# Optimization experiments

Measured on AMD Instinct MI355X. Metric: run time of the kernel, lower is better.

The kernel has to match this reference:

```python
import jax, jax.numpy as jnp
import numpy as np

NEG = -1000.0  # matches the -1000 masking used in the original module


def setup_inputs() -> dict:
    key = jax.random.key(0)
    k0, k1, k2 = jax.random.split(key, 3)
    B, L, T = 512, 512, 32
    S = T + 2  # states: 0 = START, 1..T = tags, T+1 = STOP
    word_tag_value = jax.random.normal(k0, (B, L, T), dtype=jnp.float32)
    # xavier_uniform-style init for the transition matrix, then mask per the original
    a = float(np.sqrt(6.0 / (S + S)))
    translation = jax.random.uniform(k1, (S, S), dtype=jnp.float32, minval=-a, maxval=a)
    translation = translation.at[:, 0].set(NEG)       # nothing transitions into START
    translation = translation.at[S - 1, :].set(NEG)   # nothing transitions out of STOP
    real_tag = jax.random.randint(k2, (B, L), 1, T + 1)  # tags in 1..T
    return {"word_tag_value": word_tag_value, "translation": translation,
            "real_tag": real_tag, "output_loss": 1}


def _score_path(word_tag_value, translation, real_tag, T):
    # sum of emissions at the gold tags (tags 1..T index emission column tag-1)
    emit = jnp.take_along_axis(word_tag_value, (real_tag - 1)[..., None], axis=2)[..., 0]  # [B, L]
    score_emit = emit.sum(axis=1)
    # sum of transitions along the gold path + START/STOP transitions
    score_trans = translation[real_tag[:, :-1], real_tag[:, 1:]].sum(axis=1)
    score_trans = score_trans + translation[0, real_tag[:, 0]] + translation[real_tag[:, -1], T + 1]
    return score_emit + score_trans  # [B]


def _score_total(word_tag_value, translation, T):
    # forward algorithm (logsumexp recursion) over S = T+2 states
    B, L, _ = word_tag_value.shape
    # pad emissions to S states; START/STOP get NEG emission mid-sequence
    obs = jnp.pad(word_tag_value, ((0, 0), (0, 0), (1, 1)), constant_values=NEG)  # [B, L, S]
    # initial alpha: emissions of step 0 at tag states, 0 at START/STOP (as in original)
    alpha0 = jnp.pad(word_tag_value[:, 0, :], ((0, 0), (1, 1)), constant_values=0.0)  # [B, S]

    def step(alpha, obs_t):
        # scores[prev, cur] = alpha[prev] + obs_t[cur] + translation[prev, cur]
        m = alpha[:, :, None] + obs_t[:, None, :] + translation[None, :, :]  # [B, S, S]
        return jax.nn.logsumexp(m, axis=1), None

    alpha_T, _ = jax.lax.scan(step, alpha0, jnp.swapaxes(obs, 0, 1)[1:])  # scan over L-1 steps
    return jax.nn.logsumexp(alpha_T, axis=1)  # [B]


def reference(word_tag_value, translation, real_tag, output_loss):
    T = word_tag_value.shape[-1]
    if output_loss:
        return _score_total(word_tag_value, translation, T) - _score_path(word_tag_value, translation, real_tag, T)
    return None
```

## Files before the change

### kernel.cpp

```cpp
#include <hip/hip_runtime.h>


#define F2   1.4426950408889634f
#define LN2  0.6931471805599453f
#define BIAS 0.0078125f
#define BIASCNT 3577

__global__ __launch_bounds__(64) void crf_kernel(
    const float* __restrict__ wtv,
    const float* __restrict__ trans,
    const int*   __restrict__ rtag,
    float* __restrict__ out)
{
    __shared__ __align__(16) float tlds[1156];
    __shared__ __align__(16) int   ltag[1024];
    __shared__ __align__(16) float alds[160];

    const int l = threadIdx.x;
    const int q = l >> 5;
    const int c = l & 31;
    const int bbase = blockIdx.x * 2;

    for (int k = l; k < 1156; k += 64) tlds[k] = trans[k];
    {
        const int* rtb = rtag + (size_t)bbase * 512;
        for (int k = l; k < 1024; k += 64) ltag[k] = rtb[k];
    }
    __syncthreads();

    float tcF[32], tcB[32];
    #pragma unroll
    for (int k = 0; k < 32; ++k) {
        tcF[k] = __builtin_exp2f(F2 * tlds[(k + 1) * 34 + (c + 1)]) * BIAS;
        tcB[k] = __builtin_exp2f(F2 * tlds[(c + 1) * 34 + (k + 1)]) * BIAS;
    }
    float aiF = __builtin_exp2f(F2 * tlds[c + 1]) * BIAS;

    const float* wbq = wtv + (size_t)(bbase + q) * (512 * 32);

    float stF = __builtin_exp2f(F2 * wbq[c]);
    float stB = 1.0f;
    int scF = 0, scB = 0;

    float vnF[8], vnB[8], eoF[8], eoB[8];
    #pragma unroll
    for (int j = 0; j < 8; ++j) {
        vnF[j] = wbq[(1 + j) * 32 + c];
        vnB[j] = wbq[(511 - j) * 32 + c];
    }

    float* aF = alds + q * 36;
    float* aB = alds + 80 + q * 36;
    const float4* f4 = (const float4*)aF;
    const float4* b4 = (const float4*)aB;

    float4 ra[8], rb[8];

    aF[c] = stF;
    __builtin_amdgcn_wave_barrier();
    #pragma unroll
    for (int k = 0; k < 8; ++k) ra[k] = f4[k];
    __builtin_amdgcn_wave_barrier();

    for (int t0 = 1; t0 <= 249; t0 += 8) {
        #pragma unroll
        for (int j = 0; j < 8; ++j) {
            eoF[j] = __builtin_exp2f(F2 * vnF[j]);
            eoB[j] = __builtin_exp2f(F2 * vnB[j]);
        }
        {
            const int i8 = t0 + 8;
            #pragma unroll
            for (int j = 0; j < 8; ++j) {
                vnF[j] = wbq[(i8 + j) * 32 + c];
                vnB[j] = wbq[(512 - i8 - j) * 32 + c];
            }
        }
        const bool resc = ((t0 + 7) & 15) == 0;
        #pragma unroll
        for (int j = 0; j < 8; ++j) {
            const int i = t0 + j;

            aB[c] = stB * eoB[j];
            __builtin_amdgcn_wave_barrier();
            #pragma unroll
            for (int k = 0; k < 8; ++k) rb[k] = b4[k];
            __builtin_amdgcn_wave_barrier();
            {
                float a0 = aiF, a1 = 0.0f, a2 = 0.0f, a3 = 0.0f;
                aiF = 0.0f;
                #pragma unroll
                for (int k = 0; k < 8; ++k) {
                    float4 x = ra[k];
                    a0 += x.x * tcF[4 * k + 0]; a1 += x.y * tcF[4 * k + 1];
                    a2 += x.z * tcF[4 * k + 2]; a3 += x.w * tcF[4 * k + 3];
                }
                float s = (a0 + a1) + (a2 + a3);
                stF = s * eoF[j];
            }
            if (j == 7 && resc) {
                float m = stF;
                m = fmaxf(m, __shfl_xor(m, 1));
                m = fmaxf(m, __shfl_xor(m, 2));
                m = fmaxf(m, __shfl_xor(m, 4));
                m = fmaxf(m, __shfl_xor(m, 8));
                m = fmaxf(m, __shfl_xor(m, 16));
                int e = ((__float_as_int(m) >> 23) & 0xff) - 127;
                stF *= __int_as_float((127 - e) << 23);
                scF += e;
            }

            aF[c] = stF;
            __builtin_amdgcn_wave_barrier();
            #pragma unroll
            for (int k = 0; k < 8; ++k) ra[k] = f4[k];
            __builtin_amdgcn_wave_barrier();
            {
                float a0 = 0.0f, a1 = 0.0f, a2 = 0.0f, a3 = 0.0f;
                #pragma unroll
                for (int k = 0; k < 8; ++k) {
                    float4 x = rb[k];
                    a0 += x.x * tcB[4 * k + 0]; a1 += x.y * tcB[4 * k + 1];
                    a2 += x.z * tcB[4 * k + 2]; a3 += x.w * tcB[4 * k + 3];
                }
                float s = (a0 + a1) + (a2 + a3);
                stB = (i != 256) ? s : stB;
            }
        }
        if (resc) {
            float m = stB;
            m = fmaxf(m, __shfl_xor(m, 1));
            m = fmaxf(m, __shfl_xor(m, 2));
            m = fmaxf(m, __shfl_xor(m, 4));
            m = fmaxf(m, __shfl_xor(m, 8));
            m = fmaxf(m, __shfl_xor(m, 16));
            int e = ((__float_as_int(m) >> 23) & 0xff) - 127;
            stB *= __int_as_float((127 - e) << 23);
            scB += e;
        }
    }

    float prod = stF * stB;
    prod += __shfl_xor(prod, 1);
    prod += __shfl_xor(prod, 2);
    prod += __shfl_xor(prod, 4);
    prod += __shfl_xor(prod, 8);
    prod += __shfl_xor(prod, 16);
    float total = ((float)(scF + scB + BIASCNT) + __builtin_log2f(prod)) * LN2;

    float ps0 = 0.0f, ps1 = 0.0f;
    #pragma unroll
    for (int bb = 0; bb < 2; ++bb) {
        const float* w  = wtv + (size_t)(bbase + bb) * (512 * 32);
        const int*   tg = ltag + (bb << 9);
        int   tcur[8];
        float em[8];
        #pragma unroll
        for (int k = 0; k < 8; ++k) tcur[k] = tg[l + 64 * k];
        #pragma unroll
        for (int k = 0; k < 8; ++k) em[k] = w[(l + 64 * k) * 32 + (tcur[k] - 1)];
        float acc = 0.0f;
        #pragma unroll
        for (int k = 0; k < 8; ++k) {
            int t  = l + 64 * k;
            int nx = tg[(t + 1) & 511];
            nx = (t == 511) ? 33 : nx;
            acc += em[k] + tlds[tcur[k] * 34 + nx];
        }
        if (l == 0) acc += tlds[tg[0]];
        acc += __shfl_xor(acc, 1);
        acc += __shfl_xor(acc, 2);
        acc += __shfl_xor(acc, 4);
        acc += __shfl_xor(acc, 8);
        acc += __shfl_xor(acc, 16);
        acc += __shfl_xor(acc, 32);
        if (bb == 0) ps0 = acc; else ps1 = acc;
    }
    float ps = (q == 0) ? ps0 : ps1;
    if (c == 0) out[bbase + q] = total - ps;
}

extern "C" void kernel_launch(void* const* d_in, const int* in_sizes, int n_in,
                              void* d_out, int out_size, void* d_ws, size_t ws_size,
                              hipStream_t stream) {
    const float* wtv   = (const float*)d_in[0];
    const float* trans = (const float*)d_in[1];
    const int*   rtag  = (const int*)d_in[2];
    (void)in_sizes; (void)n_in; (void)d_ws; (void)ws_size; (void)out_size;
    float* out = (float*)d_out;
    crf_kernel<<<256, 64, 0, stream>>>(wtv, trans, rtag, out);
}
```

Before: 144.9 us.

## Software-pipeline emission loads per step, unroll by 16, use DPP max reductions

Restructures the forward/backward recursion loop into 16-step blocks. Each step now prefetches the emission value eight steps ahead into a rotating 16-entry register ring and computes the next step's exp2 inside the current step, so global loads and transcendental work are spread across the dependency chain instead of issued in bursts. The per-block max reduction for rescaling uses DPP row shifts plus a ds_swizzle in place of shfl_xor, and the rescale now happens once per 16-step block with no separate resc predicate. This adds register pressure from the larger ring and full 16-way unroll, and changes how the final step is handled at t0==241.

```diff
diff --git a/kernel.cpp b/kernel.cpp
--- a/kernel.cpp
+++ b/kernel.cpp
@@ -5,6 +5,21 @@
 #define LN2  0.6931471805599453f
 #define BIAS 0.0078125f
 #define BIASCNT 3577
+
+__device__ __forceinline__ float grpmax32(float x) {
+    int t;
+    t = __builtin_amdgcn_update_dpp(__float_as_int(x), __float_as_int(x), 0x121, 0xf, 0xf, true);
+    x = fmaxf(x, __int_as_float(t));
+    t = __builtin_amdgcn_update_dpp(__float_as_int(x), __float_as_int(x), 0x122, 0xf, 0xf, true);
+    x = fmaxf(x, __int_as_float(t));
+    t = __builtin_amdgcn_update_dpp(__float_as_int(x), __float_as_int(x), 0x124, 0xf, 0xf, true);
+    x = fmaxf(x, __int_as_float(t));
+    t = __builtin_amdgcn_update_dpp(__float_as_int(x), __float_as_int(x), 0x128, 0xf, 0xf, true);
+    x = fmaxf(x, __int_as_float(t));
+    t = __builtin_amdgcn_ds_swizzle(__float_as_int(x), 0x401F);
+    x = fmaxf(x, __int_as_float(t));
+    return x;
+}
 
 __global__ __launch_bounds__(64) void crf_kernel(
     const float* __restrict__ wtv,
@@ -42,12 +57,14 @@
     float stB = 1.0f;
     int scF = 0, scB = 0;
 
-    float vnF[8], vnB[8], eoF[8], eoB[8];
+    float vnF[16], vnB[16];
     #pragma unroll
     for (int j = 0; j < 8; ++j) {
         vnF[j] = wbq[(1 + j) * 32 + c];
         vnB[j] = wbq[(511 - j) * 32 + c];
     }
+    float eoF_c = __builtin_exp2f(F2 * vnF[0]);
+    float gB    = stB * __builtin_exp2f(F2 * vnB[0]);
 
     float* aF = alds + q * 36;
     float* aB = alds + 80 + q * 36;
@@ -62,30 +79,18 @@
     for (int k = 0; k < 8; ++k) ra[k] = f4[k];
     __builtin_amdgcn_wave_barrier();
 
-    for (int t0 = 1; t0 <= 249; t0 += 8) {
+    for (int t0 = 1; t0 <= 241; t0 += 16) {
         #pragma unroll
-        for (int j = 0; j < 8; ++j) {
-            eoF[j] = __builtin_exp2f(F2 * vnF[j]);
-            eoB[j] = __builtin_exp2f(F2 * vnB[j]);
-        }
-        {
-            const int i8 = t0 + 8;
-            #pragma unroll
-            for (int j = 0; j < 8; ++j) {
-                vnF[j] = wbq[(i8 + j) * 32 + c];
-                vnB[j] = wbq[(512 - i8 - j) * 32 + c];
-            }
-        }
-        const bool resc = ((t0 + 7) & 15) == 0;
-        #pragma unroll
-        for (int j = 0; j < 8; ++j) {
+        for (int j = 0; j < 16; ++j) {
             const int i = t0 + j;
 
-            aB[c] = stB * eoB[j];
+            aB[c] = gB;
             __builtin_amdgcn_wave_barrier();
             #pragma unroll
             for (int k = 0; k < 8; ++k) rb[k] = b4[k];
             __builtin_amdgcn_wave_barrier();
+            vnB[(j + 8) & 15] = wbq[(512 - (i + 8)) * 32 + c];
+            float eoB_n = __builtin_exp2f(F2 * vnB[(j + 1) & 15]);
             {
                 float a0 = aiF, a1 = 0.0f, a2 = 0.0f, a3 = 0.0f;
                 aiF = 0.0f;
@@ -96,15 +101,10 @@
                     a2 += x.z * tcF[4 * k + 2]; a3 += x.w * tcF[4 * k + 3];
                 }
                 float s = (a0 + a1) + (a2 + a3);
-                stF = s * eoF[j];
+                stF = s * eoF_c;
             }
-            if (j == 7 && resc) {
-                float m = stF;
-                m = fmaxf(m, __shfl_xor(m, 1));
-                m = fmaxf(m, __shfl_xor(m, 2));
-                m = fmaxf(m, __shfl_xor(m, 4));
-                m = fmaxf(m, __shfl_xor(m, 8));
-                m = fmaxf(m, __shfl_xor(m, 16));
+            if (j == 15) {
+                float m = grpmax32(stF);
                 int e = ((__float_as_int(m) >> 23) & 0xff) - 127;
                 stF *= __int_as_float((127 - e) << 23);
                 scF += e;
@@ -115,6 +115,8 @@
             #pragma unroll
             for (int k = 0; k < 8; ++k) ra[k] = f4[k];
             __builtin_amdgcn_wave_barrier();
+            vnF[(j + 8) & 15] = wbq[(i + 8) * 32 + c];
+            float eoF_n = __builtin_exp2f(F2 * vnF[(j + 1) & 15]);
             {
                 float a0 = 0.0f, a1 = 0.0f, a2 = 0.0f, a3 = 0.0f;
                 #pragma unroll
@@ -124,19 +126,17 @@
                     a2 += x.z * tcB[4 * k + 2]; a3 += x.w * tcB[4 * k + 3];
                 }
                 float s = (a0 + a1) + (a2 + a3);
-                stB = (i != 256) ? s : stB;
+                if (j == 15) stB = (t0 != 241) ? s : stB;
+                else         stB = s;
             }
-        }
-        if (resc) {
-            float m = stB;
-            m = fmaxf(m, __shfl_xor(m, 1));
-            m = fmaxf(m, __shfl_xor(m, 2));
-            m = fmaxf(m, __shfl_xor(m, 4));
-            m = fmaxf(m, __shfl_xor(m, 8));
-            m = fmaxf(m, __shfl_xor(m, 16));
-            int e = ((__float_as_int(m) >> 23) & 0xff) - 127;
-            stB *= __int_as_float((127 - e) << 23);
-            scB += e;
+            if (j == 15) {
+                float m = grpmax32(stB);
+                int e = ((__float_as_int(m) >> 23) & 0xff) - 127;
+                stB *= __int_as_float((127 - e) << 23);
+                scB += e;
+            }
+            gB   = stB * eoB_n;
+            eoF_c = eoF_n;
         }
     }
 
```

Measured after the change: 139.1 us. 4.0% less time.
